# Performance work log

Hardware: AMD Instinct MI355X
Metric: run time of the kernel (lower is better)

Reference implementation:

```python
import jax, jax.numpy as jnp
import numpy as np

N_ATOMS, N_BONDS, MAX_NB = 100_000, 200_000, 6
ATOM_FDIM, BOND_FDIM = 133, 147
HIDDEN, DEPTH = 256, 3
N_MOLS, MOL_FEAT = 4096, 200
FFNN_HID, ENC_HID = 512, 256


def setup_inputs() -> dict:
    key = jax.random.key(0)
    ks = jax.random.split(key, 12)
    f_atoms = jax.random.normal(ks[0], (N_ATOMS, ATOM_FDIM), jnp.float32)
    f_bonds = jax.random.normal(ks[1], (N_BONDS, BOND_FDIM), jnp.float32)
    a2b = jax.random.randint(ks[2], (N_ATOMS, MAX_NB), 0, N_BONDS, jnp.int32)
    b2a = jax.random.randint(ks[3], (N_BONDS,), 0, N_ATOMS, jnp.int32)
    # reverse bond of directed bond i is its pair partner (i XOR 1)
    b2revb = (jnp.arange(N_BONDS, dtype=jnp.int32) ^ 1)
    atom2mol = jnp.sort(jax.random.randint(ks[4], (N_ATOMS,), 0, N_MOLS, jnp.int32))
    mol_features = jax.random.normal(ks[5], (N_MOLS, MOL_FEAT), jnp.float32)
    # weights stored as [in, out]
    W_i = jax.random.normal(ks[6], (BOND_FDIM, HIDDEN), jnp.float32) / np.sqrt(BOND_FDIM)
    W_h = jax.random.normal(ks[7], (HIDDEN, HIDDEN), jnp.float32) / np.sqrt(HIDDEN)
    W_o_w = jax.random.normal(ks[8], (ATOM_FDIM + HIDDEN, HIDDEN), jnp.float32) / np.sqrt(ATOM_FDIM + HIDDEN)
    W_o_b = jnp.zeros((HIDDEN,), jnp.float32)
    W1 = jax.random.normal(ks[9], (HIDDEN + MOL_FEAT, FFNN_HID), jnp.float32) / np.sqrt(HIDDEN + MOL_FEAT)
    b1 = jnp.zeros((FFNN_HID,), jnp.float32)
    W2 = jax.random.normal(ks[10], (FFNN_HID, ENC_HID), jnp.float32) / np.sqrt(FFNN_HID)
    b2 = jnp.zeros((ENC_HID,), jnp.float32)
    return dict(f_atoms=f_atoms, f_bonds=f_bonds, a2b=a2b, b2a=b2a, b2revb=b2revb,
                atom2mol=atom2mol, mol_features=mol_features,
                W_i=W_i, W_h=W_h, W_o_w=W_o_w, W_o_b=W_o_b,
                W1=W1, b1=b1, W2=W2, b2=b2)


def reference(f_atoms, f_bonds, a2b, b2a, b2revb, atom2mol, mol_features,
              W_i, W_h, W_o_w, W_o_b, W1, b1, W2, b2):
    n_mols = mol_features.shape[0]
    inputs = f_bonds @ W_i                      # [B, H]
    message = jax.nn.relu(inputs)
    for _ in range(DEPTH - 1):
        nei = message[a2b]                      # [A, MAX_NB, H] gather
        a_message = nei.sum(axis=1)             # [A, H]
        message = jax.nn.relu(inputs + (a_message[b2a] - message[b2revb]) @ W_h)
    nei = message[a2b]
    a_message = nei.sum(axis=1)                 # [A, H]
    a_input = jnp.concatenate([f_atoms, a_message], axis=1)
    atom_hiddens = jax.nn.relu(a_input @ W_o_w + W_o_b)  # [A, H]
    # per-molecule mean; empty molecules -> zero vector (cached_zero_vector)
    sums = jax.ops.segment_sum(atom_hiddens, atom2mol, num_segments=n_mols)
    counts = jax.ops.segment_sum(jnp.ones((atom_hiddens.shape[0],), atom_hiddens.dtype),
                                 atom2mol, num_segments=n_mols)
    mol_vecs = sums / jnp.maximum(counts, 1.0)[:, None]  # [n_mols, H]
    x = jnp.concatenate([mol_vecs, mol_features], axis=1)
    h = jax.nn.relu(x @ W1 + b1)
    out = jax.nn.relu(h @ W2 + b2)
    return out
```

## Files before the change

kernel.cpp:

```cpp
#include <hip/hip_runtime.h>
#include <hip/hip_bf16.h>


typedef __hip_bfloat16 bf16;
typedef __attribute__((ext_vector_type(8))) short short8;
typedef __attribute__((ext_vector_type(4))) short short4v;
typedef __attribute__((ext_vector_type(4))) float f32x4;
typedef __attribute__((ext_vector_type(4), aligned(4))) float f32x4u;

__device__ __forceinline__ float b2f(bf16 x) { return __bfloat162float(x); }
__device__ __forceinline__ bf16  f2b(float x) { return __float2bfloat16(x); }
__device__ __forceinline__ float bs2f(short s) {
    unsigned int u = ((unsigned int)(unsigned short)s) << 16;
    float f; __builtin_memcpy(&f, &u, 4); return f;
}
__device__ __forceinline__ short f2bs(float f) {
    bf16 b = __float2bfloat16(f);
    short s; __builtin_memcpy(&s, &b, 2); return s;
}

#define GRID 256
#define TR 32

template <int KP, int MODE, bool RELU, int ADDC, bool HASBIAS, bool OUTF32>
__global__ __launch_bounds__(512, 1) void gemm_wres(
    int M, int ntiles, int Ktrue,
    const float* __restrict__ Af,
    const bf16* __restrict__ Ab1, const bf16* __restrict__ Ab2,
    const int* __restrict__ g1, const int* __restrict__ g2,
    const bf16* __restrict__ Wt,
    const float* __restrict__ bias,
    const bf16* __restrict__ addB, const float* __restrict__ addF,
    bf16* __restrict__ outB, float* __restrict__ outF)
{
    constexpr int NK  = KP / 32;
    constexpr int NU  = KP / 8;
    constexpr int KP2 = KP * 2;
    __shared__ bf16 Wl[256 * KP];
    __shared__ bf16 At[TR * KP];

    const int t = threadIdx.x;
    int tile = blockIdx.x;
    if (tile >= ntiles) return;

    {
        int n = t >> 1, half = t & 1;
        const short8* src = (const short8*)(Wt + (size_t)n * KP) + half * (NU / 2);
        char* dst = (char*)Wl + (size_t)n * KP2;
        #pragma unroll
        for (int i = 0; i < NU / 2; i++) {
            int g = half * (NU / 2) + i;
            *(short8*)(dst + ((g ^ (n & 7)) << 4)) = src[i];
        }
    }
    __syncthreads();

    const int wave = t >> 6, lane = t & 63;
    const int mrow = lane & 15, kq = lane >> 4;
    const int r = t >> 4, j = t & 15;

    float biasReg[2] = {0.f, 0.f};
    if (HASBIAS) {
        #pragma unroll
        for (int tn = 0; tn < 2; tn++)
            biasReg[tn] = bias[wave * 32 + tn * 16 + mrow];
    }

    short8 pA[2], pB[2];
    f32x4  pF[3];
    short8 pC[2];

    auto prefA = [&](int tl) {
        int row = tl * TR + r;
        if (MODE == 1) {
            int r1 = g1[row], r2 = g2[row];
            const char* s1 = (const char*)(Ab1 + ((size_t)r1 << 8));
            const char* s2 = (const char*)(Ab2 + ((size_t)r2 << 8));
            #pragma unroll
            for (int u = 0; u < 2; u++) {
                pA[u] = *(const short8*)(s1 + ((j + 16 * u) << 4));
                pB[u] = *(const short8*)(s2 + ((j + 16 * u) << 4));
            }
        } else if (MODE == 2) {
            const char* s1 = (const char*)(Ab1 + ((size_t)row << 8));
            #pragma unroll
            for (int u = 0; u < 2; u++)
                pA[u] = *(const short8*)(s1 + ((j + 16 * u) << 4));
        } else {
            const float* src = Af + (size_t)row * Ktrue;
            #pragma unroll
            for (int v = 0; v < 3; v++) {
                int c = j + 16 * v;
                f32x4 val = {0.f, 0.f, 0.f, 0.f};
                if (c * 4 < Ktrue) {
                    if (row == M - 1 && c * 4 + 4 > Ktrue) {
                        #pragma unroll
                        for (int e = 0; e < 4; e++)
                            if (c * 4 + e < Ktrue) val[e] = src[c * 4 + e];
                    } else {
                        val = *(const f32x4u*)(src + c * 4);
                    }
                }
                pF[v] = val;
            }
        }
    };
    auto prefAdd = [&](int tl) {
        int row = tl * TR + r;
        const char* s = (const char*)(addB + ((size_t)row << 8));
        #pragma unroll
        for (int u = 0; u < 2; u++)
            pC[u] = *(const short8*)(s + ((j + 16 * u) << 4));
    };
    auto convWrite = [&]() {
        char* dst = (char*)At + (size_t)r * KP2;
        if (MODE == 1) {
            #pragma unroll
            for (int u = 0; u < 2; u++) {
                short8 a = pA[u], b = pB[u], o;
                #pragma unroll
                for (int e = 0; e < 8; e++)
                    o[e] = f2bs(bs2f(a[e]) - fmaxf(bs2f(b[e]), 0.f));
                int g = j + 16 * u;
                *(short8*)(dst + ((g ^ (r & 7)) << 4)) = o;
            }
        } else if (MODE == 2) {
            #pragma unroll
            for (int u = 0; u < 2; u++) {
                int g = j + 16 * u;
                *(short8*)(dst + ((g ^ (r & 7)) << 4)) = pA[u];
            }
        } else {
            #pragma unroll
            for (int v = 0; v < 3; v++) {
                int c = j + 16 * v;
                f32x4 x = pF[v];
                short4v o;
                #pragma unroll
                for (int e = 0; e < 4; e++) o[e] = f2bs(x[e]);
                int unit = c >> 1, sub = (c & 1) << 3;
                *(short4v*)(dst + ((unit ^ (r & 7)) << 4) + sub) = o;
            }
        }
    };

    prefA(tile);
    for (;;) {
        convWrite();
        __syncthreads();
        const int nxt = tile + GRID;
        const bool more = nxt < ntiles;
        if (ADDC == 1) prefAdd(tile);
        if (more) prefA(nxt);

        f32x4 acc[2][2] = {};
        #pragma unroll
        for (int ks = 0; ks < NK; ks++) {
            short8 afr[2], bfr[2];
            #pragma unroll
            for (int tm = 0; tm < 2; tm++) {
                int arow = tm * 16 + mrow;
                afr[tm] = *(const short8*)((char*)At + (size_t)arow * KP2 +
                            (((ks * 4 + kq) ^ (arow & 7)) << 4));
            }
            #pragma unroll
            for (int tn = 0; tn < 2; tn++) {
                int n = wave * 32 + tn * 16 + mrow;
                bfr[tn] = *(const short8*)((char*)Wl + (size_t)n * KP2 +
                            (((ks * 4 + kq) ^ (n & 7)) << 4));
            }
            #pragma unroll
            for (int tm = 0; tm < 2; tm++)
                #pragma unroll
                for (int tn = 0; tn < 2; tn++)
                    acc[tm][tn] = __builtin_amdgcn_mfma_f32_16x16x32_bf16(
                        afr[tm], bfr[tn], acc[tm][tn], 0, 0, 0);
        }
        __syncthreads();

        if (ADDC == 1) {
            char* dst = (char*)At + (size_t)r * KP2;
            #pragma unroll
            for (int u = 0; u < 2; u++) {
                int g = j + 16 * u;
                *(short8*)(dst + ((g ^ (r & 7)) << 4)) = pC[u];
            }
            __syncthreads();
        }

        const int bm = tile * TR;
        #pragma unroll
        for (int tm = 0; tm < 2; tm++) {
            #pragma unroll
            for (int rr = 0; rr < 4; rr++) {
                int lrow = tm * 16 + kq * 4 + rr;
                size_t rb = (size_t)(bm + lrow) << 8;
                #pragma unroll
                for (int tn = 0; tn < 2; tn++) {
                    int col = wave * 32 + tn * 16 + mrow;
                    float v = acc[tm][tn][rr];
                    if (HASBIAS) v += biasReg[tn];
                    if (ADDC == 1) {
                        int u = col >> 3;
                        short s = *(const short*)((char*)At + (size_t)lrow * KP2 +
                                   ((u ^ (lrow & 7)) << 4) + ((col & 7) << 1));
                        v += bs2f(s);
                    } else if (ADDC == 2) {
                        v += addF[rb + col];
                    }
                    if (RELU) v = fmaxf(v, 0.f);
                    if (OUTF32) outF[rb + col] = v;
                    else        outB[rb + col] = f2b(v);
                }
            }
        }
        if (!more) break;
        if (ADDC == 1) __syncthreads();
        tile = nxt;
    }
}

__global__ __launch_bounds__(256) void convert_wt(
    const float* __restrict__ W, bf16* __restrict__ Wt, int K, int Koff, int Kp)
{
    int i = blockIdx.x * 256 + threadIdx.x;
    if (i >= 256 * Kp) return;
    int n = i / Kp, k = i - n * Kp;
    Wt[i] = (k < K) ? f2b(W[(size_t)(k + Koff) * 256 + n]) : f2b(0.f);
}

__global__ __launch_bounds__(256) void gather_sum4(
    const bf16* __restrict__ msg, const int* __restrict__ a2b,
    bf16* __restrict__ amsg, int A)
{
    int idx = blockIdx.x * 256 + threadIdx.x;
    if (idx >= A * 64) return;
    int a  = idx >> 6;
    int c4 = (idx & 63) * 4;
    const int* nb = a2b + (size_t)a * 6;
    float s0 = 0.f, s1 = 0.f, s2 = 0.f, s3 = 0.f;
    #pragma unroll
    for (int k = 0; k < 6; k++) {
        const short4v v = *(const short4v*)(msg + (size_t)nb[k] * 256 + c4);
        s0 += fmaxf(bs2f(v[0]), 0.f);
        s1 += fmaxf(bs2f(v[1]), 0.f);
        s2 += fmaxf(bs2f(v[2]), 0.f);
        s3 += fmaxf(bs2f(v[3]), 0.f);
    }
    short4v o; o[0] = f2bs(s0); o[1] = f2bs(s1); o[2] = f2bs(s2); o[3] = f2bs(s3);
    *(short4v*)(amsg + (size_t)a * 256 + c4) = o;
}

__global__ __launch_bounds__(256) void segment_mean_kernel(
    const bf16* __restrict__ ah, const int* __restrict__ atom2mol,
    int A, float* __restrict__ molv)
{
    int m = blockIdx.x;
    int h = threadIdx.x;
    int lo = 0, hi = A;
    while (lo < hi) { int mid = (lo + hi) >> 1; if (atom2mol[mid] < m) lo = mid + 1; else hi = mid; }
    int start = lo;
    hi = A;
    while (lo < hi) { int mid = (lo + hi) >> 1; if (atom2mol[mid] <= m) lo = mid + 1; else hi = mid; }
    int end = lo;
    float s = 0.f;
    for (int a = start; a < end; a++) s += b2f(ah[(size_t)a * 256 + h]);
    float cnt = (float)(end - start);
    molv[(size_t)m * 256 + h] = s / fmaxf(cnt, 1.f);
}

#define TM 64
#define TN 64
#define TK 16
__global__ __launch_bounds__(256) void gemm_f32(
    int M, int N, int K, int K1,
    const float* __restrict__ Af1,
    const float* __restrict__ Af2,
    const float* __restrict__ W,
    const float* __restrict__ bias,
    float* __restrict__ outF)
{
    __shared__ float As[TK][TM + 4];
    __shared__ float Bs[TK][TN + 4];
    const int bm = blockIdx.x * TM;
    const int bn = blockIdx.y * TN;
    const int t  = threadIdx.x;
    const int tx = t & 15;
    const int ty = t >> 4;
    float acc[4][4] = {};
    for (int k0 = 0; k0 < K; k0 += TK) {
        #pragma unroll
        for (int i = 0; i < 4; i++) {
            int idx = t + i * 256;
            int rr = idx >> 4, kk = idx & 15;
            int rowi = bm + rr, k = k0 + kk;
            float v = 0.f;
            if (rowi < M && k < K)
                v = (k < K1) ? Af1[(size_t)rowi * K1 + k]
                             : Af2[(size_t)rowi * (K - K1) + (k - K1)];
            As[kk][rr] = v;
        }
        #pragma unroll
        for (int i = 0; i < 4; i++) {
            int idx = t + i * 256;
            int nn = idx & 63, kk = idx >> 6;
            int k = k0 + kk, n = bn + nn;
            float v = 0.f;
            if (k < K && n < N) v = W[(size_t)k * N + n];
            Bs[kk][nn] = v;
        }
        __syncthreads();
        #pragma unroll
        for (int kk = 0; kk < TK; kk++) {
            float a[4], b[4];
            #pragma unroll
            for (int i = 0; i < 4; i++) a[i] = As[kk][ty * 4 + i];
            #pragma unroll
            for (int jj = 0; jj < 4; jj++) b[jj] = Bs[kk][tx * 4 + jj];
            #pragma unroll
            for (int i = 0; i < 4; i++)
                #pragma unroll
                for (int jj = 0; jj < 4; jj++)
                    acc[i][jj] += a[i] * b[jj];
        }
        __syncthreads();
    }
    #pragma unroll
    for (int i = 0; i < 4; i++) {
        int rowi = bm + ty * 4 + i;
        if (rowi >= M) continue;
        #pragma unroll
        for (int jj = 0; jj < 4; jj++) {
            int n = bn + tx * 4 + jj;
            if (n >= N) continue;
            float v = acc[i][jj] + (bias ? bias[n] : 0.f);
            outF[(size_t)rowi * N + n] = fmaxf(v, 0.f);
        }
    }
}

extern "C" void kernel_launch(void* const* d_in, const int* in_sizes, int n_in,
                              void* d_out, int out_size, void* d_ws, size_t ws_size,
                              hipStream_t stream)
{
    const float* f_atoms  = (const float*)d_in[0];
    const float* f_bonds  = (const float*)d_in[1];
    const int*   a2b      = (const int*)d_in[2];
    const int*   b2a      = (const int*)d_in[3];
    const int*   b2revb   = (const int*)d_in[4];
    const int*   atom2mol = (const int*)d_in[5];
    const float* mol_feat = (const float*)d_in[6];
    const float* W_i      = (const float*)d_in[7];
    const float* W_h      = (const float*)d_in[8];
    const float* W_o_w    = (const float*)d_in[9];
    const float* W_o_b    = (const float*)d_in[10];
    const float* W1       = (const float*)d_in[11];
    const float* b1       = (const float*)d_in[12];
    const float* W2       = (const float*)d_in[13];
    const float* b2       = (const float*)d_in[14];

    const int A  = 100000, B = 200000, H = 256;
    const int AF = 133, BF = 147;
    const int NM = 4096, MF = 200, FH = 512, EH = 256;
    const int KpS = 192;
    const int KpH = 256;

    char* ws = (char*)d_ws;
    bf16* buf0 = (bf16*)ws;  ws += (size_t)B * H * sizeof(bf16);
    bf16* buf1 = (bf16*)ws;  ws += (size_t)B * H * sizeof(bf16);
    bf16* amsg = (bf16*)ws;  ws += (size_t)A * H * sizeof(bf16);
    float* molv = (float*)ws; ws += (size_t)NM * H * sizeof(float);
    float* hbuf = (float*)ws; ws += (size_t)NM * FH * sizeof(float);
    bf16* WtI  = (bf16*)ws;  ws += (size_t)256 * KpS * sizeof(bf16);
    bf16* WtH  = (bf16*)ws;  ws += (size_t)256 * KpH * sizeof(bf16);
    bf16* WtO1 = (bf16*)ws;  ws += (size_t)256 * KpS * sizeof(bf16);
    bf16* WtO2 = (bf16*)ws;  ws += (size_t)256 * KpH * sizeof(bf16);
    float* fbuf = (float*)buf1;

    dim3 blk(256), blkG(512);
    const int ntB = B / TR;
    const int ntA = A / TR;
    const int gsG = (A * 64 + 255) / 256;

    convert_wt<<<dim3((256 * KpS + 255) / 256), blk, 0, stream>>>(W_i,   WtI,  BF,  0,  KpS);
    convert_wt<<<dim3((256 * KpH + 255) / 256), blk, 0, stream>>>(W_h,   WtH,  H,   0,  KpH);
    convert_wt<<<dim3((256 * KpS + 255) / 256), blk, 0, stream>>>(W_o_w, WtO1, AF,  0,  KpS);
    convert_wt<<<dim3((256 * KpH + 255) / 256), blk, 0, stream>>>(W_o_w, WtO2, H,   AF, KpH);

    gemm_wres<192, 0, false, 0, false, false><<<dim3(GRID), blkG, 0, stream>>>(
        B, ntB, BF, f_bonds, nullptr, nullptr, nullptr, nullptr,
        WtI, nullptr, nullptr, nullptr, buf0, nullptr);

    gather_sum4<<<dim3(gsG), blk, 0, stream>>>(buf0, a2b, amsg, A);
    gemm_wres<256, 1, true, 1, false, false><<<dim3(GRID), blkG, 0, stream>>>(
        B, ntB, H, nullptr, amsg, buf0, b2a, b2revb,
        WtH, nullptr, buf0, nullptr, buf1, nullptr);

    gather_sum4<<<dim3(gsG), blk, 0, stream>>>(buf1, a2b, amsg, A);
    gemm_wres<256, 1, true, 1, false, false><<<dim3(GRID), blkG, 0, stream>>>(
        B, ntB, H, nullptr, amsg, buf1, b2a, b2revb,
        WtH, nullptr, buf0, nullptr, buf0, nullptr);

    gather_sum4<<<dim3(gsG), blk, 0, stream>>>(buf0, a2b, amsg, A);

    gemm_wres<192, 0, false, 0, false, true><<<dim3(GRID), blkG, 0, stream>>>(
        A, ntA, AF, f_atoms, nullptr, nullptr, nullptr, nullptr,
        WtO1, nullptr, nullptr, nullptr, nullptr, fbuf);

    gemm_wres<256, 2, true, 2, true, false><<<dim3(GRID), blkG, 0, stream>>>(
        A, ntA, H, nullptr, amsg, nullptr, nullptr, nullptr,
        WtO2, W_o_b, nullptr, fbuf, amsg, nullptr);

    segment_mean_kernel<<<dim3(NM), blk, 0, stream>>>(amsg, atom2mol, A, molv);

    gemm_f32<<<dim3((NM + TM - 1) / TM, FH / TN), blk, 0, stream>>>(
        NM, FH, H + MF, H, molv, mol_feat, W1, b1, hbuf);

    gemm_f32<<<dim3((NM + TM - 1) / TM, EH / TN), blk, 0, stream>>>(
        NM, EH, FH, FH, hbuf, nullptr, W2, b2, (float*)d_out);
}
```

Baseline: 824.5 us.

## Replace FP32 FFN GEMMs with split-bf16 MFMA GEMMs and widen gather vectors

```diff
diff --git a/kernel.cpp b/kernel.cpp
--- a/kernel.cpp
+++ b/kernel.cpp
@@ -229,112 +229,175 @@
     Wt[i] = (k < K) ? f2b(W[(size_t)(k + Koff) * 256 + n]) : f2b(0.f);
 }
 
-__global__ __launch_bounds__(256) void gather_sum4(
+__global__ __launch_bounds__(256) void gather_sum8(
     const bf16* __restrict__ msg, const int* __restrict__ a2b,
     bf16* __restrict__ amsg, int A)
 {
     int idx = blockIdx.x * 256 + threadIdx.x;
-    if (idx >= A * 64) return;
-    int a  = idx >> 6;
-    int c4 = (idx & 63) * 4;
+    if (idx >= A * 32) return;
+    int a  = idx >> 5;
+    int c8 = (idx & 31) * 8;
     const int* nb = a2b + (size_t)a * 6;
-    float s0 = 0.f, s1 = 0.f, s2 = 0.f, s3 = 0.f;
+    float s[8] = {};
     #pragma unroll
     for (int k = 0; k < 6; k++) {
-        const short4v v = *(const short4v*)(msg + (size_t)nb[k] * 256 + c4);
-        s0 += fmaxf(bs2f(v[0]), 0.f);
-        s1 += fmaxf(bs2f(v[1]), 0.f);
-        s2 += fmaxf(bs2f(v[2]), 0.f);
-        s3 += fmaxf(bs2f(v[3]), 0.f);
-    }
-    short4v o; o[0] = f2bs(s0); o[1] = f2bs(s1); o[2] = f2bs(s2); o[3] = f2bs(s3);
-    *(short4v*)(amsg + (size_t)a * 256 + c4) = o;
-}
-
-__global__ __launch_bounds__(256) void segment_mean_kernel(
+        const short8 v = *(const short8*)(msg + ((size_t)nb[k] << 8) + c8);
+        #pragma unroll
+        for (int e = 0; e < 8; e++) s[e] += fmaxf(bs2f(v[e]), 0.f);
+    }
+    short8 o;
+    #pragma unroll
+    for (int e = 0; e < 8; e++) o[e] = f2bs(s[e]);
+    *(short8*)(amsg + ((size_t)a << 8) + c8) = o;
+}
+
+#define K3 1536
+
+__global__ __launch_bounds__(256) void conv_w3(
+    const float* __restrict__ W, bf16* __restrict__ Wp, int K, int N)
+{
+    int idx = blockIdx.x * 256 + threadIdx.x;
+    if (idx >= N * 512) return;
+    int n = idx >> 9, k = idx & 511;
+    float w = (k < K) ? W[(size_t)k * N + n] : 0.f;
+    bf16 hi = f2b(w);
+    bf16 lo = f2b(w - b2f(hi));
+    size_t base = (size_t)n * K3;
+    Wp[base + k] = hi;
+    Wp[base + 512 + k] = hi;
+    Wp[base + 1024 + k] = lo;
+}
+
+__global__ __launch_bounds__(256) void conv_feat(
+    const float* __restrict__ mf, bf16* __restrict__ A1p)
+{
+    int idx = blockIdx.x * 256 + threadIdx.x;
+    int m = idx >> 8, j = idx & 255;
+    float v = (j < 200) ? mf[(size_t)m * 200 + j] : 0.f;
+    bf16 hi = f2b(v);
+    bf16 lo = f2b(v - b2f(hi));
+    size_t base = (size_t)m * K3 + 256;
+    A1p[base + j] = hi;
+    A1p[base + 512 + j] = lo;
+    A1p[base + 1024 + j] = hi;
+}
+
+__global__ __launch_bounds__(256) void segment_mean3(
     const bf16* __restrict__ ah, const int* __restrict__ atom2mol,
-    int A, float* __restrict__ molv)
+    int A, bf16* __restrict__ A1p)
 {
     int m = blockIdx.x;
     int h = threadIdx.x;
-    int lo = 0, hi = A;
-    while (lo < hi) { int mid = (lo + hi) >> 1; if (atom2mol[mid] < m) lo = mid + 1; else hi = mid; }
-    int start = lo;
-    hi = A;
-    while (lo < hi) { int mid = (lo + hi) >> 1; if (atom2mol[mid] <= m) lo = mid + 1; else hi = mid; }
-    int end = lo;
+    int lo_ = 0, hi_ = A;
+    while (lo_ < hi_) { int mid = (lo_ + hi_) >> 1; if (atom2mol[mid] < m) lo_ = mid + 1; else hi_ = mid; }
+    int start = lo_;
+    hi_ = A;
+    while (lo_ < hi_) { int mid = (lo_ + hi_) >> 1; if (atom2mol[mid] <= m) lo_ = mid + 1; else hi_ = mid; }
+    int end = lo_;
     float s = 0.f;
     for (int a = start; a < end; a++) s += b2f(ah[(size_t)a * 256 + h]);
-    float cnt = (float)(end - start);
-    molv[(size_t)m * 256 + h] = s / fmaxf(cnt, 1.f);
-}
-
-#define TM 64
-#define TN 64
-#define TK 16
-__global__ __launch_bounds__(256) void gemm_f32(
-    int M, int N, int K, int K1,
-    const float* __restrict__ Af1,
-    const float* __restrict__ Af2,
-    const float* __restrict__ W,
+    float mean = s / fmaxf((float)(end - start), 1.f);
+    bf16 hi = f2b(mean);
+    bf16 lo = f2b(mean - b2f(hi));
+    size_t base = (size_t)m * K3;
+    A1p[base + h] = hi;
+    A1p[base + 512 + h] = lo;
+    A1p[base + 1024 + h] = hi;
+}
+
+template <bool OUT3>
+__global__ __launch_bounds__(256, 2) void gemm3(
+    int N,
+    const bf16* __restrict__ Ap, const bf16* __restrict__ Wp,
     const float* __restrict__ bias,
-    float* __restrict__ outF)
-{
-    __shared__ float As[TK][TM + 4];
-    __shared__ float Bs[TK][TN + 4];
-    const int bm = blockIdx.x * TM;
-    const int bn = blockIdx.y * TN;
-    const int t  = threadIdx.x;
-    const int tx = t & 15;
-    const int ty = t >> 4;
-    float acc[4][4] = {};
-    for (int k0 = 0; k0 < K; k0 += TK) {
-        #pragma unroll
-        for (int i = 0; i < 4; i++) {
-            int idx = t + i * 256;
-            int rr = idx >> 4, kk = idx & 15;
-            int rowi = bm + rr, k = k0 + kk;
-            float v = 0.f;
-            if (rowi < M && k < K)
-                v = (k < K1) ? Af1[(size_t)rowi * K1 + k]
-                             : Af2[(size_t)rowi * (K - K1) + (k - K1)];
-            As[kk][rr] = v;
-        }
-        #pragma unroll
-        for (int i = 0; i < 4; i++) {
-            int idx = t + i * 256;
-            int nn = idx & 63, kk = idx >> 6;
-            int k = k0 + kk, n = bn + nn;
-            float v = 0.f;
-            if (k < K && n < N) v = W[(size_t)k * N + n];
-            Bs[kk][nn] = v;
-        }
+    bf16* __restrict__ out3, float* __restrict__ outF)
+{
+    __shared__ bf16 As[2][64 * 64];
+    __shared__ bf16 Bs[2][64 * 64];
+
+    const int t = threadIdx.x;
+    const int bm = blockIdx.x * 64, bn = blockIdx.y * 64;
+    const int row = t >> 2, q = t & 3;
+    const bf16* srcA = Ap + (size_t)(bm + row) * K3 + q * 16;
+    const bf16* srcB = Wp + (size_t)(bn + row) * K3 + q * 16;
+
+    short8 ra[2], rb[2];
+    auto LOADT = [&](int t0) {
+        #pragma unroll
+        for (int u = 0; u < 2; u++) {
+            ra[u] = *(const short8*)(srcA + t0 * 64 + u * 8);
+            rb[u] = *(const short8*)(srcB + t0 * 64 + u * 8);
+        }
+    };
+    auto WRITET = [&](int buf) {
+        char* da = (char*)&As[buf][0] + row * 128;
+        char* db = (char*)&Bs[buf][0] + row * 128;
+        #pragma unroll
+        for (int u = 0; u < 2; u++) {
+            int g = q * 2 + u;
+            *(short8*)(da + ((g ^ (row & 7)) << 4)) = ra[u];
+            *(short8*)(db + ((g ^ (row & 7)) << 4)) = rb[u];
+        }
+    };
+
+    const int wave = t >> 6, lane = t & 63;
+    const int mrow = lane & 15, kq = lane >> 4;
+    const int wm = (wave >> 1) * 32, wn = (wave & 1) * 32;
+
+    f32x4 acc[2][2] = {};
+    LOADT(0);
+    WRITET(0);
+
+    for (int t0 = 0; t0 < K3 / 64; t0++) {
+        const int cur = t0 & 1;
         __syncthreads();
-        #pragma unroll
-        for (int kk = 0; kk < TK; kk++) {
-            float a[4], b[4];
-            #pragma unroll
-            for (int i = 0; i < 4; i++) a[i] = As[kk][ty * 4 + i];
-            #pragma unroll
-            for (int jj = 0; jj < 4; jj++) b[jj] = Bs[kk][tx * 4 + jj];
-            #pragma unroll
-            for (int i = 0; i < 4; i++)
+        if (t0 + 1 < K3 / 64) LOADT(t0 + 1);
+        #pragma unroll
+        for (int ks = 0; ks < 2; ks++) {
+            short8 af[2], bfr[2];
+            #pragma unroll
+            for (int i = 0; i < 2; i++) {
+                int ar = wm + i * 16 + mrow;
+                af[i] = *(const short8*)((char*)&As[cur][0] + ar * 128 +
+                          (((ks * 4 + kq) ^ (ar & 7)) << 4));
+            }
+            #pragma unroll
+            for (int jx = 0; jx < 2; jx++) {
+                int br = wn + jx * 16 + mrow;
+                bfr[jx] = *(const short8*)((char*)&Bs[cur][0] + br * 128 +
+                          (((ks * 4 + kq) ^ (br & 7)) << 4));
+            }
+            #pragma unroll
+            for (int i = 0; i < 2; i++)
                 #pragma unroll
-                for (int jj = 0; jj < 4; jj++)
-                    acc[i][jj] += a[i] * b[jj];
-        }
-        __syncthreads();
-    }
+                for (int jx = 0; jx < 2; jx++)
+                    acc[i][jx] = __builtin_amdgcn_mfma_f32_16x16x32_bf16(
+                        af[i], bfr[jx], acc[i][jx], 0, 0, 0);
+        }
+        if (t0 + 1 < K3 / 64) WRITET(cur ^ 1);
+    }
+
     #pragma unroll
-    for (int i = 0; i < 4; i++) {
-        int rowi = bm + ty * 4 + i;
-        if (rowi >= M) continue;
-        #pragma unroll
-        for (int jj = 0; jj < 4; jj++) {
-            int n = bn + tx * 4 + jj;
-            if (n >= N) continue;
-            float v = acc[i][jj] + (bias ? bias[n] : 0.f);
-            outF[(size_t)rowi * N + n] = fmaxf(v, 0.f);
+    for (int i = 0; i < 2; i++) {
+        #pragma unroll
+        for (int r = 0; r < 4; r++) {
+            int grow = bm + wm + i * 16 + kq * 4 + r;
+            #pragma unroll
+            for (int jx = 0; jx < 2; jx++) {
+                int gcol = bn + wn + jx * 16 + mrow;
+                float v = acc[i][jx][r] + bias[gcol];
+                v = fmaxf(v, 0.f);
+                if (OUT3) {
+                    bf16 hi = f2b(v);
+                    bf16 lo = f2b(v - b2f(hi));
+                    size_t base = (size_t)grow * K3;
+                    out3[base + gcol] = hi;
+                    out3[base + 512 + gcol] = lo;
+                    out3[base + 1024 + gcol] = hi;
+                } else {
+                    outF[(size_t)grow * N + gcol] = v;
+                }
+            }
         }
     }
 }
@@ -361,7 +424,7 @@
 
     const int A  = 100000, B = 200000, H = 256;
     const int AF = 133, BF = 147;
-    const int NM = 4096, MF = 200, FH = 512, EH = 256;
+    const int NM = 4096, FH = 512, EH = 256;
     const int KpS = 192;
     const int KpH = 256;
 
@@ -369,39 +432,45 @@
     bf16* buf0 = (bf16*)ws;  ws += (size_t)B * H * sizeof(bf16);
     bf16* buf1 = (bf16*)ws;  ws += (size_t)B * H * sizeof(bf16);
     bf16* amsg = (bf16*)ws;  ws += (size_t)A * H * sizeof(bf16);
-    float* molv = (float*)ws; ws += (size_t)NM * H * sizeof(float);
-    float* hbuf = (float*)ws; ws += (size_t)NM * FH * sizeof(float);
     bf16* WtI  = (bf16*)ws;  ws += (size_t)256 * KpS * sizeof(bf16);
     bf16* WtH  = (bf16*)ws;  ws += (size_t)256 * KpH * sizeof(bf16);
     bf16* WtO1 = (bf16*)ws;  ws += (size_t)256 * KpS * sizeof(bf16);
     bf16* WtO2 = (bf16*)ws;  ws += (size_t)256 * KpH * sizeof(bf16);
+    bf16* W1p  = (bf16*)ws;  ws += (size_t)FH * K3 * sizeof(bf16);
+    bf16* W2p  = (bf16*)ws;  ws += (size_t)EH * K3 * sizeof(bf16);
     float* fbuf = (float*)buf1;
+    bf16* A1p = buf0;
+    bf16* A2p = buf0 + (size_t)NM * K3;
 
     dim3 blk(256), blkG(512);
     const int ntB = B / TR;
     const int ntA = A / TR;
-    const int gsG = (A * 64 + 255) / 256;
+    const int gsG = (A * 32 + 255) / 256;
 
     convert_wt<<<dim3((256 * KpS + 255) / 256), blk, 0, stream>>>(W_i,   WtI,  BF,  0,  KpS);
     convert_wt<<<dim3((256 * KpH + 255) / 256), blk, 0, stream>>>(W_h,   WtH,  H,   0,  KpH);
     convert_wt<<<dim3((256 * KpS + 255) / 256), blk, 0, stream>>>(W_o_w, WtO1, AF,  0,  KpS);
     convert_wt<<<dim3((256 * KpH + 255) / 256), blk, 0, stream>>>(W_o_w, WtO2, H,   AF, KpH);
+    conv_w3<<<dim3((FH * 512 + 255) / 256), blk, 0, stream>>>(W1, W1p, H + 200, FH);
+    conv_w3<<<dim3((EH * 512 + 255) / 256), blk, 0, stream>>>(W2, W2p, FH, EH);
 
     gemm_wres<192, 0, false, 0, false, false><<<dim3(GRID), blkG, 0, stream>>>(
         B, ntB, BF, f_bonds, nullptr, nullptr, nullptr, nullptr,
         WtI, nullptr, nullptr, nullptr, buf0, nullptr);
 
-    gather_sum4<<<dim3(gsG), blk, 0, stream>>>(buf0, a2b, amsg, A);
+    gather_sum8<<<dim3(gsG), blk, 0, stream>>>(buf0, a2b, amsg, A);
     gemm_wres<256, 1, true, 1, false, false><<<dim3(GRID), blkG, 0, stream>>>(
         B, ntB, H, nullptr, amsg, buf0, b2a, b2revb,
         WtH, nullptr, buf0, nullptr, buf1, nullptr);
 
-    gather_sum4<<<dim3(gsG), blk, 0, stream>>>(buf1, a2b, amsg, A);
+    gather_sum8<<<dim3(gsG), blk, 0, stream>>>(buf1, a2b, amsg, A);
     gemm_wres<256, 1, true, 1, false, false><<<dim3(GRID), blkG, 0, stream>>>(
         B, ntB, H, nullptr, amsg, buf1, b2a, b2revb,
         WtH, nullptr, buf0, nullptr, buf0, nullptr);
 
-    gather_sum4<<<dim3(gsG), blk, 0, stream>>>(buf0, a2b, amsg, A);
+    gather_sum8<<<dim3(gsG), blk, 0, stream>>>(buf0, a2b, amsg, A);
+
+    conv_feat<<<dim3(NM), blk, 0, stream>>>(mol_feat, A1p);
 
     gemm_wres<192, 0, false, 0, false, true><<<dim3(GRID), blkG, 0, stream>>>(
         A, ntA, AF, f_atoms, nullptr, nullptr, nullptr, nullptr,
@@ -411,11 +480,11 @@
         A, ntA, H, nullptr, amsg, nullptr, nullptr, nullptr,
         WtO2, W_o_b, nullptr, fbuf, amsg, nullptr);
 
-    segment_mean_kernel<<<dim3(NM), blk, 0, stream>>>(amsg, atom2mol, A, molv);
-
-    gemm_f32<<<dim3((NM + TM - 1) / TM, FH / TN), blk, 0, stream>>>(
-        NM, FH, H + MF, H, molv, mol_feat, W1, b1, hbuf);
-
-    gemm_f32<<<dim3((NM + TM - 1) / TM, EH / TN), blk, 0, stream>>>(
-        NM, EH, FH, FH, hbuf, nullptr, W2, b2, (float*)d_out);
-}
+    segment_mean3<<<dim3(NM), blk, 0, stream>>>(amsg, atom2mol, A, A1p);
+
+    gemm3<true><<<dim3(NM / 64, FH / 64), blk, 0, stream>>>(
+        FH, A1p, W1p, b1, A2p, nullptr);
+
+    gemm3<false><<<dim3(NM / 64, EH / 64), blk, 0, stream>>>(
+        EH, A2p, W2p, b2, nullptr, (float*)d_out);
+}
```

After: 696.7 us. 15.5% less time.
